# Kernel tuning notes

Measured on AMD Instinct MI355X. Metric: run time of the kernel, lower is better.

## Reference

```python
import jax, jax.numpy as jnp
import numpy as np

D = 768        # TEXT_DIM
N = 50         # seq len (h,w = 1,50 in source)
HEADS = 8
LABEL_SIZE = 50
B = 512
EPS_COS = 1e-8
EPS_LN = 1e-5


def _egce(x, w):
    # EGCE source not provided in repo snippet; implemented as ECA-style efficient
    # gated channel excitation: GAP over HW -> 1D conv (k=3) over channels -> sigmoid gate.
    gap = x.mean(axis=(2, 3))                      # [b, c]
    p = jnp.pad(gap, ((0, 0), (1, 1)))
    att = jax.nn.sigmoid(w[0] * p[:, :-2] + w[1] * p[:, 1:-1] + w[2] * p[:, 2:])
    return x * att[:, :, None, None]


def _lstm(x, Wih, Whh, bih, bhh):
    # PyTorch single-layer batch_first LSTM, gate order i,f,g,o, zero init state.
    b, n, d = x.shape
    xg = jnp.einsum('bnd,gd->bng', x, Wih) + bih + bhh   # [b, n, 4d]
    def step(carry, xt):
        h, c = carry
        g = xt + h @ Whh.T
        i, f, gg, o = jnp.split(g, 4, axis=-1)
        c = jax.nn.sigmoid(f) * c + jax.nn.sigmoid(i) * jnp.tanh(gg)
        h = jax.nn.sigmoid(o) * jnp.tanh(c)
        return (h, c), h
    h0 = jnp.zeros((b, d), x.dtype)
    _, ys = jax.lax.scan(step, (h0, h0), jnp.swapaxes(xg, 0, 1))
    return jnp.swapaxes(ys, 0, 1)


def _cross_attn(q_in, kv_in, qW, qb, kW, kb, vW, vb):
    b, n, d = q_in.shape
    dh = d // HEADS
    q = (q_in @ qW.T + qb).reshape(b, n, HEADS, dh).transpose(0, 2, 1, 3)
    k = (kv_in @ kW.T + kb).reshape(b, -1, HEADS, dh).transpose(0, 2, 1, 3)
    v = (kv_in @ vW.T + vb).reshape(b, -1, HEADS, dh).transpose(0, 2, 1, 3)
    attn = jax.nn.softmax(jnp.einsum('bhqd,bhkd->bhqk', q, k) * dh ** -0.5, axis=-1)
    # NOTE: faithful to source: einsum('bhqk,bhvd->bhqd') sums k and v INDEPENDENTLY
    out = jnp.einsum('bhqk,bhvd->bhqd', attn, v)
    return out.transpose(0, 2, 1, 3).reshape(b, n, d)


def _ln(x, g, b):
    m = x.mean(-1, keepdims=True)
    v = ((x - m) ** 2).mean(-1, keepdims=True)
    return (x - m) * jax.lax.rsqrt(v + EPS_LN) * g + b


def setup_inputs() -> dict:
    key = jax.random.key(0)
    ks = jax.random.split(key, 24)
    s = 0.02
    def w(k, shape):
        return jax.random.normal(k, shape, jnp.float32) * s
    vis_emb = w(ks[0], (LABEL_SIZE + 1, D)).at[LABEL_SIZE].set(0.0)
    ac_emb = w(ks[1], (LABEL_SIZE + 1, D)).at[LABEL_SIZE].set(0.0)
    inp = {
        'text_embedding': jax.random.normal(ks[2], (B, N, D), jnp.float32),
        'visual_ids': jax.random.randint(ks[3], (B, N), 0, LABEL_SIZE),
        'acoustic_ids': jax.random.randint(ks[4], (B, N), 0, LABEL_SIZE),
        'vis_emb': vis_emb,
        'ac_emb': ac_emb,
        'egce_w': w(ks[5], (3,)) + 0.3,
        'lstm_Wih': w(ks[6], (4 * D, D)),
        'lstm_Whh': w(ks[7], (4 * D, D)),
        'lstm_bih': jnp.zeros((4 * D,), jnp.float32),
        'lstm_bhh': jnp.zeros((4 * D,), jnp.float32),
        'ln_g': jnp.ones((D,), jnp.float32),
        'ln_b': jnp.zeros((D,), jnp.float32),
        'concat_W': w(ks[8], (D, 3 * D)),
        'concat_b': jnp.zeros((D,), jnp.float32),
        'hybrid_W': w(ks[9], (D, 3 * D)),
        'hybrid_b': jnp.zeros((D,), jnp.float32),
        # stacked cross-attention params, index 0 = cross_att_t, 1 = cross_att_a, 2 = cross_att_v
        'ca_qW': w(ks[10], (3, D, D)), 'ca_qb': w(ks[11], (3, D)),
        'ca_kW': w(ks[12], (3, D, D)), 'ca_kb': w(ks[13], (3, D)),
        'ca_vW': w(ks[14], (3, D, D)), 'ca_vb': w(ks[15], (3, D)),
    }
    return inp


def _forward(text_embedding, vis_emb, ac_emb, egce_w, lstm_Wih, lstm_Whh,
             lstm_bih, lstm_bhh, ln_g, ln_b, concat_W, concat_b, hybrid_W,
             hybrid_b, ca_qW, ca_qb, ca_kW, ca_kb, ca_vW, ca_vb,
             visual_ids, acoustic_ids):
    b, n, c = text_embedding.shape
    visual_ = jax.nn.relu(vis_emb[visual_ids])
    acoustic_ = ac_emb[acoustic_ids]
    # faithful reshape (NOT transpose) [b,n,c] -> [b,c,1,n] -> egce -> [b,n,c]
    text = _egce(text_embedding.reshape(b, c, 1, n), egce_w).reshape(b, n, c)
    visual_ = _egce(visual_.reshape(b, c, 1, n), egce_w).reshape(b, n, c)
    acoustic_ = _egce(acoustic_.reshape(b, c, 1, n), egce_w).reshape(b, n, c)

    # ---- AFI (vectorized over batch via masks instead of Python loop) ----
    def cos(x, y):
        xm, ym = x.mean(1), y.mean(1)
        nx = jnp.maximum(jnp.sqrt((xm * xm).sum(-1)), EPS_COS)
        ny = jnp.maximum(jnp.sqrt((ym * ym).sum(-1)), EPS_COS)
        return (xm * ym).sum(-1) / (nx * ny)
    rtv, rta, rva = cos(text, visual_), cos(text, acoustic_), cos(visual_, acoustic_)
    delta = (rtv + rta + rva) / 3.0
    joint = (rtv + rta + rva) / 3.0   # identical to delta in source
    cat = jnp.concatenate([text, visual_, acoustic_], axis=-1)  # [b,n,3d]
    f_concat = cat @ concat_W.T + concat_b
    f_hybrid = cat @ hybrid_W.T + hybrid_b
    tv = _cross_attn(text, visual_, ca_qW[0], ca_qb[0], ca_kW[0], ca_kb[0], ca_vW[0], ca_vb[0])
    ta = _cross_attn(text, acoustic_, ca_qW[1], ca_qb[1], ca_kW[1], ca_kb[1], ca_vW[1], ca_vb[1])
    va = _cross_attn(visual_, acoustic_, ca_qW[2], ca_qb[2], ca_kW[2], ca_kb[2], ca_vW[2], ca_vb[2])
    f_cross = (tv + ta + va) / 3.0
    m1 = ((rtv > delta) & (rta > delta) & (rva > delta))[:, None, None]
    m2 = (joint > delta)[:, None, None]
    fusion = jnp.where(m1, f_concat, jnp.where(m2, f_hybrid, f_cross))
    # dropout is identity in eval mode

    shift = _ln(fusion + text, ln_g, ln_b)
    out = _lstm(shift, lstm_Wih, lstm_Whh, lstm_bih, lstm_bhh) + text
    return out


def reference(text_embedding, visual_ids, acoustic_ids, vis_emb, ac_emb, egce_w,
              lstm_Wih, lstm_Whh, lstm_bih, lstm_bhh, ln_g, ln_b, concat_W,
              concat_b, hybrid_W, hybrid_b, ca_qW, ca_qb, ca_kW, ca_kb, ca_vW, ca_vb):
    return _forward(text_embedding, vis_emb, ac_emb, egce_w, lstm_Wih, lstm_Whh,
                    lstm_bih, lstm_bhh, ln_g, ln_b, concat_W, concat_b, hybrid_W,
                    hybrid_b, ca_qW, ca_qb, ca_kW, ca_kb, ca_vW, ca_vb,
                    visual_ids, acoustic_ids)
```

## Files before the change

kernel.cpp:

```cpp
#include <hip/hip_runtime.h>
#include <hip/hip_bf16.h>
#include <math.h>

#define B 512
#define N 50
#define D 768
#define G4 3072
#define BN (B*N)
#define FLAT (N*D)
#define TCH 10
#define NCHUNK (N/TCH)
#define KC 1536
#define CCH 6400

typedef __hip_bfloat16 bf16;
typedef short short8 __attribute__((ext_vector_type(8)));
typedef float floatx4 __attribute__((ext_vector_type(4)));

__device__ __forceinline__ float sigf(float x){ return 1.0f/(1.0f+expf(-x)); }
__device__ __forceinline__ float u2f(unsigned short u){ return __uint_as_float(((unsigned int)u)<<16); }
__device__ __forceinline__ unsigned short f2u(float f){ bf16 h=__float2bfloat16(f); return *(unsigned short*)&h; }

#define GLD16(g,l) __builtin_amdgcn_global_load_lds( \
    (const __attribute__((address_space(1))) unsigned int*)(g), \
    (__attribute__((address_space(3))) unsigned int*)(l), 16, 0, 0)

__global__ __launch_bounds__(256) void egce_fused(
    const float* __restrict__ text, const int* __restrict__ vid, const int* __restrict__ aid,
    const float* __restrict__ vemb, const float* __restrict__ aemb, const float* __restrict__ egw,
    float* __restrict__ att_t, unsigned short* __restrict__ catAB){
  __shared__ float buf[CCH];
  __shared__ float gt[D+2], gv[D+2], ga[D+2];
  __shared__ float attvS[D], attaS[D];
  __shared__ int vidS[N], aidS[N];
  int b=blockIdx.x, tid=threadIdx.x;
  if(tid<N){ vidS[tid]=vid[b*N+tid]; aidS[tid]=aid[b*N+tid]; }
  if(tid==0){ gt[0]=gv[0]=ga[0]=0.f; gt[D+1]=gv[D+1]=ga[D+1]=0.f; }
  __syncthreads();
  const float* tb = text + (size_t)b*FLAT;
  for(int c=0;c<6;c++){
    int j0=c*CCH;
    for(int it=0;it<25;it++) buf[it*256+tid]=tb[j0+it*256+tid];
    __syncthreads();
    if(tid<128){ float s=0.f; for(int p=0;p<50;p++) s+=buf[tid*50+p]; gt[c*128+tid+1]=s*(1.f/50.f); }
    __syncthreads();
    for(int it=0;it<25;it++){ int j=j0+it*256+tid; int n=j/D, d=j-n*D;
      float v=vemb[vidS[n]*D+d]; buf[it*256+tid]=v>0.f?v:0.f; }
    __syncthreads();
    if(tid<128){ float s=0.f; for(int p=0;p<50;p++) s+=buf[tid*50+p]; gv[c*128+tid+1]=s*(1.f/50.f); }
    __syncthreads();
    for(int it=0;it<25;it++){ int j=j0+it*256+tid; int n=j/D, d=j-n*D;
      buf[it*256+tid]=aemb[aidS[n]*D+d]; }
    __syncthreads();
    if(tid<128){ float s=0.f; for(int p=0;p<50;p++) s+=buf[tid*50+p]; ga[c*128+tid+1]=s*(1.f/50.f); }
    __syncthreads();
  }
  float w0=egw[0],w1=egw[1],w2=egw[2];
  for(int ch=tid;ch<D;ch+=256){
    att_t[(size_t)b*D+ch]=sigf(w0*gt[ch]+w1*gt[ch+1]+w2*gt[ch+2]);
    attvS[ch]=sigf(w0*gv[ch]+w1*gv[ch+1]+w2*gv[ch+2]);
    attaS[ch]=sigf(w0*ga[ch]+w1*ga[ch+1]+w2*ga[ch+2]);
  }
  __syncthreads();
  float va[3]={0,0,0}, aa[3]={0,0,0};
  for(int n=0;n<N;n++){
    int idv=vidS[n], ida=aidS[n];
    #pragma unroll
    for(int q=0;q<3;q++){
      int d=q*256+tid;
      int ch=(n*D+d)/50;
      float vv=vemb[idv*D+d]; vv=vv>0.f?vv:0.f;
      va[q]+=vv*attvS[ch];
      aa[q]+=aemb[ida*D+d]*attaS[ch];
    }
  }
  for(int q=0;q<3;q++){
    int d=q*256+tid;
    catAB[(size_t)b*KC+d]    =f2u(va[q]);
    catAB[(size_t)b*KC+D+d]  =f2u(aa[q]);
  }
}

__global__ __launch_bounds__(256) void prep_weights(
    const float* __restrict__ Wih, const float* __restrict__ Whh,
    const float* __restrict__ bih, const float* __restrict__ bhh,
    unsigned short* __restrict__ WihP, unsigned short* __restrict__ WhhP,
    float* __restrict__ bsum){
  int np = blockIdx.x;
  int dg = np>>2, g = np&3;
  size_t src = (size_t)(g*D+dg)*D;
  for(int k=threadIdx.x;k<D;k+=256){
    WihP[(size_t)np*D+k] = f2u(Wih[src+k]);
    WhhP[(size_t)np*D+k] = f2u(Whh[src+k]);
  }
  if(threadIdx.x==0) bsum[np] = bih[g*D+dg] + bhh[g*D+dg];
}

__global__ __launch_bounds__(256) void prep_fcross(
    const float* __restrict__ vW, const float* __restrict__ vb,
    unsigned short* __restrict__ WcB, float* __restrict__ fb){
  int n = blockIdx.x;
  const float* W0 = vW; const float* W1 = vW + D*D; const float* W2 = vW + 2*D*D;
  for(int k=threadIdx.x;k<D;k+=256){
    WcB[(size_t)n*KC + k]     = f2u(W0[(size_t)n*D+k]);
    WcB[(size_t)n*KC + D + k] = f2u(W1[(size_t)n*D+k] + W2[(size_t)n*D+k]);
  }
  if(threadIdx.x==0) fb[n] = 50.f*(vb[n]+vb[D+n]+vb[2*D+n]);
}

__global__ __launch_bounds__(256) void fcross_mfma(
    const unsigned short* __restrict__ catAB, const unsigned short* __restrict__ WcB,
    const float* __restrict__ fb, float* __restrict__ fcross){
  __shared__ unsigned short Ash[32*40];
  __shared__ unsigned short Bsh[64*40];
  int tid=threadIdx.x;
  int bx=blockIdx.x, by=blockIdx.y;
  int lane=tid&63, w=tid>>6;
  int l15=lane&15, lq=lane>>4;
  int arow=tid>>3, aseg=(tid&7)*4;
  int brow=tid>>2, bseg=(tid&3)*8;
  floatx4 acc0={},acc1={};
  const unsigned short* aG = catAB + (size_t)(by*32 + arow)*KC + aseg;
  const unsigned short* bG = WcB   + (size_t)(bx*64 + brow)*KC + bseg;
  for(int k0=0;k0<KC;k0+=32){
    *(uint2*)&Ash[arow*40 + aseg] = *(const uint2*)(aG + k0);
    *(uint4*)&Bsh[brow*40 + bseg] = *(const uint4*)(bG + k0);
    __syncthreads();
    short8 a0=*(const short8*)&Ash[l15*40 + lq*8];
    short8 a1=*(const short8*)&Ash[(16+l15)*40 + lq*8];
    short8 bb=*(const short8*)&Bsh[(w*16 + l15)*40 + lq*8];
    acc0=__builtin_amdgcn_mfma_f32_16x16x32_bf16(a0,bb,acc0,0,0,0);
    acc1=__builtin_amdgcn_mfma_f32_16x16x32_bf16(a1,bb,acc1,0,0,0);
    __syncthreads();
  }
  int n = bx*64 + w*16 + l15;
  float bias = fb[n];
  #pragma unroll
  for(int r=0;r<4;r++){
    int m0 = by*32 + lq*4 + r;
    fcross[(size_t)m0*D + n]      = (acc0[r] + bias)*(1.f/3.f);
    fcross[(size_t)(m0+16)*D + n] = (acc1[r] + bias)*(1.f/3.f);
  }
}

__global__ __launch_bounds__(256) void fuse_ln(
    const float* __restrict__ text, const float* __restrict__ att_t,
    const float* __restrict__ fcross, const float* __restrict__ lng,
    const float* __restrict__ lnb, bf16* __restrict__ shift){
  int row = blockIdx.x;
  int b = row/N, n = row - b*N;
  int tid=threadIdx.x;
  float v[3];
  for(int q=0;q<3;q++){
    int d=q*256+tid;
    int ch=(n*D+d)/50;
    v[q] = text[(size_t)row*D+d]*att_t[(size_t)b*D+ch] + fcross[(size_t)b*D+d];
  }
  __shared__ float red[256];
  red[tid]=v[0]+v[1]+v[2]; __syncthreads();
  for(int st=128;st>0;st>>=1){ if(tid<st) red[tid]+=red[tid+st]; __syncthreads(); }
  float m = red[0]*(1.f/768.f);
  __syncthreads();
  float s2=0.f;
  for(int q=0;q<3;q++){ float dl=v[q]-m; s2+=dl*dl; }
  red[tid]=s2; __syncthreads();
  for(int st=128;st>0;st>>=1){ if(tid<st) red[tid]+=red[tid+st]; __syncthreads(); }
  float var = red[0]*(1.f/768.f);
  float rs = 1.f/sqrtf(var+1e-5f);
  for(int q=0;q<3;q++){
    int d=q*256+tid;
    shift[(size_t)row*D+d]=__float2bfloat16((v[q]-m)*rs*lng[d]+lnb[d]);
  }
}

__global__ __launch_bounds__(256) void zero_init(float* __restrict__ cbuf, unsigned short* __restrict__ h0){
  size_t i=(size_t)blockIdx.x*256+threadIdx.x;
  if(i<(size_t)B*D){ cbuf[i]=0.f; h0[i]=0; }
}

__global__ __launch_bounds__(256) void xg_gemm_m97(
    const unsigned short* __restrict__ shift, const unsigned short* __restrict__ WihP,
    const float* __restrict__ bsum, unsigned short* __restrict__ xgc, int c0){
  __shared__ unsigned short Ash[128*32];
  __shared__ unsigned short Bsh[128*32];
  int tid=threadIdx.x;
  int bx=blockIdx.x, by=blockIdx.y;
  int lane=tid&63, w=tid>>6;
  int wm=w&1, wn=w>>1;
  int l15=lane&15, lq=lane>>4;
  int srow=tid>>2, scol=(tid&3)*8;
  int R0 = by*128 + srow;
  int b0 = R0/TCH, t0 = R0 - b0*TCH;
  int R1 = R0 + 64;
  int b1 = R1/TCH, t1 = R1 - b1*TCH;
  const unsigned short* aG0 = shift + ((size_t)b0*N + c0 + t0)*D + scol;
  const unsigned short* aG1 = shift + ((size_t)b1*N + c0 + t1)*D + scol;
  const unsigned short* bG0 = WihP + (size_t)(bx*128 + srow)*D + scol;
  const unsigned short* bG1 = WihP + (size_t)(bx*128 + srow + 64)*D + scol;
  unsigned short* aL0 = &Ash[srow*32 + scol];
  unsigned short* aL1 = &Ash[(srow+64)*32 + scol];
  unsigned short* bL0 = &Bsh[srow*32 + scol];
  unsigned short* bL1 = &Bsh[(srow+64)*32 + scol];
  floatx4 acc[4][4]={};
  for(int k0=0;k0<D;k0+=32){
    GLD16(aG0+k0, aL0);
    GLD16(aG1+k0, aL1);
    GLD16(bG0+k0, bL0);
    GLD16(bG1+k0, bL1);
    __syncthreads();
    short8 af[4], bf[4];
    #pragma unroll
    for(int i=0;i<4;i++){
      af[i]=*(const short8*)&Ash[(wm*64 + i*16 + l15)*32 + lq*8];
      bf[i]=*(const short8*)&Bsh[(wn*64 + i*16 + l15)*32 + lq*8];
    }
    #pragma unroll
    for(int mi=0;mi<4;mi++)
      #pragma unroll
      for(int ni=0;ni<4;ni++)
        acc[mi][ni]=__builtin_amdgcn_mfma_f32_16x16x32_bf16(af[mi],bf[ni],acc[mi][ni],0,0,0);
    __syncthreads();
  }
  #pragma unroll
  for(int ni=0;ni<4;ni++){
    int n = bx*128 + wn*64 + ni*16 + l15;
    float bs = bsum[n];
    #pragma unroll
    for(int mi=0;mi<4;mi++){
      #pragma unroll
      for(int r=0;r<4;r++){
        size_t m = (size_t)by*128 + wm*64 + mi*16 + lq*4 + r;
        xgc[m*G4 + n] = f2u(acc[mi][ni][r] + bs);
      }
    }
  }
}

__global__ __launch_bounds__(256) void lstm_step_mfma(
    const unsigned short* __restrict__ hprev, unsigned short* __restrict__ hnext,
    float* __restrict__ cbuf, const unsigned short* __restrict__ xgc,
    const unsigned short* __restrict__ WhhP,
    const float* __restrict__ text, const float* __restrict__ att_t,
    float* __restrict__ out, int t, int tin){
  __shared__ unsigned short Ash[32*40];
  __shared__ unsigned short Bsh[64*40];
  __shared__ float gbuf[32][65];
  int tid=threadIdx.x;
  int bx=blockIdx.x, by=blockIdx.y;
  int lane=tid&63, w=tid>>6;
  int l15=lane&15, lq=lane>>4;
  int arow=tid>>3, aseg=(tid&7)*4;
  int brow=tid>>2, bseg=(tid&3)*8;
  floatx4 acc0={},acc1={};
  const unsigned short* aG = hprev + (size_t)(by*32 + arow)*D + aseg;
  const unsigned short* bG = WhhP + (size_t)(bx*64 + brow)*D + bseg;
  for(int k0=0;k0<D;k0+=32){
    *(uint2*)&Ash[arow*40 + aseg] = *(const uint2*)(aG + k0);
    *(uint4*)&Bsh[brow*40 + bseg] = *(const uint4*)(bG + k0);
    __syncthreads();
    short8 a0=*(const short8*)&Ash[l15*40 + lq*8];
    short8 a1=*(const short8*)&Ash[(16+l15)*40 + lq*8];
    short8 bb=*(const short8*)&Bsh[(w*16 + l15)*40 + lq*8];
    acc0=__builtin_amdgcn_mfma_f32_16x16x32_bf16(a0,bb,acc0,0,0,0);
    acc1=__builtin_amdgcn_mfma_f32_16x16x32_bf16(a1,bb,acc1,0,0,0);
    __syncthreads();
  }
  {
    int n = w*16 + l15;
    #pragma unroll
    for(int r=0;r<4;r++){
      gbuf[lq*4+r][n]      = acc0[r];
      gbuf[16+lq*4+r][n]   = acc1[r];
    }
  }
  __syncthreads();
  for(int p=tid;p<512;p+=256){
    int bl=p>>4, dgl=p&15;
    int b=by*32+bl, dg=bx*16+dgl;
    size_t xr=((size_t)b*TCH + tin)*G4 + bx*64 + dgl*4;
    float gi=gbuf[bl][dgl*4+0] + u2f(xgc[xr+0]);
    float gf=gbuf[bl][dgl*4+1] + u2f(xgc[xr+1]);
    float gg=gbuf[bl][dgl*4+2] + u2f(xgc[xr+2]);
    float go=gbuf[bl][dgl*4+3] + u2f(xgc[xr+3]);
    float c_old=cbuf[(size_t)b*D+dg];
    float cn=sigf(gf)*c_old + sigf(gi)*tanhf(gg);
    float hn=sigf(go)*tanhf(cn);
    cbuf[(size_t)b*D+dg]=cn;
    hnext[(size_t)b*D+dg]=f2u(hn);
    size_t oidx=((size_t)b*N+t)*D+dg;
    int ch=(t*D+dg)/50;
    out[oidx]=hn + text[oidx]*att_t[(size_t)b*D+ch];
  }
}

extern "C" void kernel_launch(void* const* d_in, const int* in_sizes, int n_in,
                              void* d_out, int out_size, void* d_ws, size_t ws_size,
                              hipStream_t stream){
  const float* text=(const float*)d_in[0];
  const int*  vid =(const int*) d_in[1];
  const int*  aid =(const int*) d_in[2];
  const float* vemb=(const float*)d_in[3];
  const float* aemb=(const float*)d_in[4];
  const float* egw =(const float*)d_in[5];
  const float* Wih =(const float*)d_in[6];
  const float* Whh =(const float*)d_in[7];
  const float* bih =(const float*)d_in[8];
  const float* bhh =(const float*)d_in[9];
  const float* lng =(const float*)d_in[10];
  const float* lnb =(const float*)d_in[11];
  const float* vW  =(const float*)d_in[20];
  const float* vb  =(const float*)d_in[21];
  float* out = (float*)d_out;

  float* W = (float*)d_ws;
  const size_t S = (size_t)B*D;
  float* att_t = W;
  float* fcross= att_t + S;
  float* cbuf  = fcross + S;
  float* bsum  = cbuf + S;
  float* fb    = bsum + G4;
  unsigned short* WihP = (unsigned short*)(fb + D);
  unsigned short* WhhP = WihP + (size_t)G4*D;
  unsigned short* WcB  = WhhP + (size_t)G4*D;
  unsigned short* catAB= WcB + (size_t)D*KC;
  unsigned short* hA0  = catAB + (size_t)B*KC;
  unsigned short* hA1  = hA0 + S;
  bf16*  shift = (bf16*)(hA1 + S);
  unsigned short* xgc  = (unsigned short*)(shift + (size_t)BN*D);

  prep_weights<<<G4,256,0,stream>>>(Wih,Whh,bih,bhh,WihP,WhhP,bsum);
  prep_fcross<<<D,256,0,stream>>>(vW,vb,WcB,fb);
  egce_fused<<<B,256,0,stream>>>(text,vid,aid,vemb,aemb,egw,att_t,catAB);
  fcross_mfma<<<dim3(12,16),256,0,stream>>>(catAB,WcB,fb,fcross);
  fuse_ln<<<BN,256,0,stream>>>(text,att_t,fcross,lng,lnb,shift);
  zero_init<<<(unsigned)((S+255)/256),256,0,stream>>>(cbuf,hA0);

  int t=0;
  for(int c=0;c<NCHUNK;c++){
    xg_gemm_m97<<<dim3(24, 40),256,0,stream>>>((const unsigned short*)shift,WihP,bsum,xgc,c*TCH);
    for(int ti=0;ti<TCH;ti++,t++){
      unsigned short* hp = (t&1)? hA1 : hA0;
      unsigned short* hn = (t&1)? hA0 : hA1;
      lstm_step_mfma<<<dim3(48,16),256,0,stream>>>(hp,hn,cbuf,xgc,WhhP,text,att_t,out,t,ti);
    }
  }
}
```

Baseline: 1.252 ms.

## Replace per-step LSTM launches with persistent kernel using grid barrier

Measured after the change: 2.381 ms. +90.1%, slower.

```diff
diff --git a/kernel.cpp b/kernel.cpp
--- a/kernel.cpp
+++ b/kernel.cpp
@@ -8,8 +8,6 @@
 #define G4 3072
 #define BN (B*N)
 #define FLAT (N*D)
-#define TCH 10
-#define NCHUNK (N/TCH)
 #define KC 1536
 #define CCH 6400
 
@@ -20,10 +18,6 @@
 __device__ __forceinline__ float sigf(float x){ return 1.0f/(1.0f+expf(-x)); }
 __device__ __forceinline__ float u2f(unsigned short u){ return __uint_as_float(((unsigned int)u)<<16); }
 __device__ __forceinline__ unsigned short f2u(float f){ bf16 h=__float2bfloat16(f); return *(unsigned short*)&h; }
-
-#define GLD16(g,l) __builtin_amdgcn_global_load_lds( \
-    (const __attribute__((address_space(1))) unsigned int*)(g), \
-    (__attribute__((address_space(3))) unsigned int*)(l), 16, 0, 0)
 
 __global__ __launch_bounds__(256) void egce_fused(
     const float* __restrict__ text, const int* __restrict__ vid, const int* __restrict__ aid,
@@ -173,123 +167,140 @@
   }
 }
 
-__global__ __launch_bounds__(256) void zero_init(float* __restrict__ cbuf, unsigned short* __restrict__ h0){
-  size_t i=(size_t)blockIdx.x*256+threadIdx.x;
-  if(i<(size_t)B*D){ cbuf[i]=0.f; h0[i]=0; }
-}
-
-__global__ __launch_bounds__(256) void xg_gemm_m97(
+__global__ __launch_bounds__(256) void zero_bar(int* __restrict__ bar){
+  bar[threadIdx.x] = 0;
+}
+
+__global__ __launch_bounds__(512) void lstm_persist(
     const unsigned short* __restrict__ shift, const unsigned short* __restrict__ WihP,
-    const float* __restrict__ bsum, unsigned short* __restrict__ xgc, int c0){
-  __shared__ unsigned short Ash[128*32];
-  __shared__ unsigned short Bsh[128*32];
-  int tid=threadIdx.x;
-  int bx=blockIdx.x, by=blockIdx.y;
-  int lane=tid&63, w=tid>>6;
-  int wm=w&1, wn=w>>1;
-  int l15=lane&15, lq=lane>>4;
-  int srow=tid>>2, scol=(tid&3)*8;
-  int R0 = by*128 + srow;
-  int b0 = R0/TCH, t0 = R0 - b0*TCH;
-  int R1 = R0 + 64;
-  int b1 = R1/TCH, t1 = R1 - b1*TCH;
-  const unsigned short* aG0 = shift + ((size_t)b0*N + c0 + t0)*D + scol;
-  const unsigned short* aG1 = shift + ((size_t)b1*N + c0 + t1)*D + scol;
-  const unsigned short* bG0 = WihP + (size_t)(bx*128 + srow)*D + scol;
-  const unsigned short* bG1 = WihP + (size_t)(bx*128 + srow + 64)*D + scol;
-  unsigned short* aL0 = &Ash[srow*32 + scol];
-  unsigned short* aL1 = &Ash[(srow+64)*32 + scol];
-  unsigned short* bL0 = &Bsh[srow*32 + scol];
-  unsigned short* bL1 = &Bsh[(srow+64)*32 + scol];
-  floatx4 acc[4][4]={};
-  for(int k0=0;k0<D;k0+=32){
-    GLD16(aG0+k0, aL0);
-    GLD16(aG1+k0, aL1);
-    GLD16(bG0+k0, bL0);
-    GLD16(bG1+k0, bL1);
-    __syncthreads();
-    short8 af[4], bf[4];
+    const unsigned short* __restrict__ WhhP, const float* __restrict__ bsum,
+    const float* __restrict__ text, const float* __restrict__ att_t,
+    unsigned short* __restrict__ h0b, unsigned short* __restrict__ h1b,
+    float* __restrict__ out, int* __restrict__ bar){
+  __shared__ unsigned short Wsl[2*2*3840];
+  const int tid = threadIdx.x;
+  const int bid = blockIdx.x;
+  const int k8 = bid & 7, u = bid >> 3;
+  const int gy = u & 7;
+  const int gx = (u >> 3) + (k8 << 2);
+  const int lane = tid & 63, w = tid >> 6;
+  const int wn = w & 1, wm = w >> 1;
+  const int l15 = lane & 15, lq = lane >> 4;
+
+  const int arrA = (tid < 384) ? 0 : 1;
+  const int sA   = (tid < 384) ? tid : tid - 384;
+  const int rlA = sA >> 2, cA = sA & 3;
+  const unsigned short* srcA = (arrA ? WihP : WhhP) + (size_t)(gx*96 + rlA)*D + cA*8;
+  const int dA = arrA*3840 + rlA*40 + cA*8;
+  const bool hasB = (tid < 256);
+  const int sB = tid + 128;
+  const int rlB = sB >> 2, cB = sB & 3;
+  const unsigned short* srcB = WihP + (size_t)(gx*96 + rlB)*D + cB*8;
+  const int dB = 3840 + rlB*40 + cB*8;
+
+  const int mrow = gy*64 + wm*16 + l15;
+  int rdh[3], rdi[3];
+  #pragma unroll
+  for(int fi=0;fi<3;fi++){
+    int rl = wn*48 + fi*16 + l15;
+    rdh[fi] = rl*40 + lq*8;
+    rdi[fi] = 3840 + rl*40 + lq*8;
+  }
+  int dgv[3]; floatx4 bs[3];
+  #pragma unroll
+  for(int fi=0;fi<3;fi++){
+    int nb = gx*96 + wn*48 + fi*16 + lq*4;
+    dgv[fi] = nb >> 2;
+    bs[fi] = *(const floatx4*)&bsum[nb];
+  }
+
+  float cst[3] = {0.f, 0.f, 0.f};
+
+  #pragma unroll 1
+  for(int t=0;t<50;++t){
+    const unsigned short* hR = (t&1) ? h1b : h0b;
+    unsigned short* hW = (t&1) ? h0b : h1b;
+    const unsigned short* sP = shift + ((size_t)mrow*N + t)*D + lq*8;
+    const unsigned short* hP = hR + (size_t)mrow*D + lq*8;
+
+    floatx4 acc[3] = {};
+
+    uint4 rA = *(const uint4*)(srcA);
+    uint4 rB = {}; if(hasB) rB = *(const uint4*)(srcB);
+    short8 sfC = *(const short8*)(sP);
+    short8 hfC = {}; if(t) hfC = *(const short8*)(hP);
+    *(uint4*)&Wsl[dA] = rA;
+    if(hasB) *(uint4*)&Wsl[dB] = rB;
+    __syncthreads();
+
     #pragma unroll
-    for(int i=0;i<4;i++){
-      af[i]=*(const short8*)&Ash[(wm*64 + i*16 + l15)*32 + lq*8];
-      bf[i]=*(const short8*)&Bsh[(wn*64 + i*16 + l15)*32 + lq*8];
+    for(int kk=0;kk<24;++kk){
+      const int bo = (kk&1)*7680;
+      uint4 nA = {}; uint4 nB = {}; short8 sfN = {}; short8 hfN = {};
+      if(kk < 23){
+        nA = *(const uint4*)(srcA + (kk+1)*32);
+        if(hasB) nB = *(const uint4*)(srcB + (kk+1)*32);
+        sfN = *(const short8*)(sP + (kk+1)*32);
+        if(t) hfN = *(const short8*)(hP + (kk+1)*32);
+      }
+      #pragma unroll
+      for(int fi=0;fi<3;fi++){
+        short8 wi = *(const short8*)&Wsl[bo + rdi[fi]];
+        acc[fi] = __builtin_amdgcn_mfma_f32_16x16x32_bf16(wi, sfC, acc[fi], 0,0,0);
+      }
+      if(t){
+        #pragma unroll
+        for(int fi=0;fi<3;fi++){
+          short8 wh = *(const short8*)&Wsl[bo + rdh[fi]];
+          acc[fi] = __builtin_amdgcn_mfma_f32_16x16x32_bf16(wh, hfC, acc[fi], 0,0,0);
+        }
+      }
+      if(kk < 23){
+        const int nx = 7680 - bo;
+        *(uint4*)&Wsl[nx + dA] = nA;
+        if(hasB) *(uint4*)&Wsl[nx + dB] = nB;
+        sfC = sfN; hfC = hfN;
+      }
+      __syncthreads();
     }
+
+    size_t tb = ((size_t)mrow*N + t)*D;
     #pragma unroll
-    for(int mi=0;mi<4;mi++)
-      #pragma unroll
-      for(int ni=0;ni<4;ni++)
-        acc[mi][ni]=__builtin_amdgcn_mfma_f32_16x16x32_bf16(af[mi],bf[ni],acc[mi][ni],0,0,0);
-    __syncthreads();
-  }
-  #pragma unroll
-  for(int ni=0;ni<4;ni++){
-    int n = bx*128 + wn*64 + ni*16 + l15;
-    float bs = bsum[n];
-    #pragma unroll
-    for(int mi=0;mi<4;mi++){
-      #pragma unroll
-      for(int r=0;r<4;r++){
-        size_t m = (size_t)by*128 + wm*64 + mi*16 + lq*4 + r;
-        xgc[m*G4 + n] = f2u(acc[mi][ni][r] + bs);
-      }
+    for(int fi=0;fi<3;fi++){
+      float gi = acc[fi][0] + bs[fi][0];
+      float gf = acc[fi][1] + bs[fi][1];
+      float gg = acc[fi][2] + bs[fi][2];
+      float go = acc[fi][3] + bs[fi][3];
+      float cn = sigf(gf)*cst[fi] + sigf(gi)*tanhf(gg);
+      float hn = sigf(go)*tanhf(cn);
+      cst[fi] = cn;
+      int dg = dgv[fi];
+      hW[(size_t)mrow*D + dg] = f2u(hn);
+      int ch = (t*D + dg)/50;
+      out[tb + dg] = hn + text[tb + dg]*att_t[(size_t)mrow*D + ch];
     }
-  }
-}
-
-__global__ __launch_bounds__(256) void lstm_step_mfma(
-    const unsigned short* __restrict__ hprev, unsigned short* __restrict__ hnext,
-    float* __restrict__ cbuf, const unsigned short* __restrict__ xgc,
-    const unsigned short* __restrict__ WhhP,
-    const float* __restrict__ text, const float* __restrict__ att_t,
-    float* __restrict__ out, int t, int tin){
-  __shared__ unsigned short Ash[32*40];
-  __shared__ unsigned short Bsh[64*40];
-  __shared__ float gbuf[32][65];
-  int tid=threadIdx.x;
-  int bx=blockIdx.x, by=blockIdx.y;
-  int lane=tid&63, w=tid>>6;
-  int l15=lane&15, lq=lane>>4;
-  int arow=tid>>3, aseg=(tid&7)*4;
-  int brow=tid>>2, bseg=(tid&3)*8;
-  floatx4 acc0={},acc1={};
-  const unsigned short* aG = hprev + (size_t)(by*32 + arow)*D + aseg;
-  const unsigned short* bG = WhhP + (size_t)(bx*64 + brow)*D + bseg;
-  for(int k0=0;k0<D;k0+=32){
-    *(uint2*)&Ash[arow*40 + aseg] = *(const uint2*)(aG + k0);
-    *(uint4*)&Bsh[brow*40 + bseg] = *(const uint4*)(bG + k0);
-    __syncthreads();
-    short8 a0=*(const short8*)&Ash[l15*40 + lq*8];
-    short8 a1=*(const short8*)&Ash[(16+l15)*40 + lq*8];
-    short8 bb=*(const short8*)&Bsh[(w*16 + l15)*40 + lq*8];
-    acc0=__builtin_amdgcn_mfma_f32_16x16x32_bf16(a0,bb,acc0,0,0,0);
-    acc1=__builtin_amdgcn_mfma_f32_16x16x32_bf16(a1,bb,acc1,0,0,0);
-    __syncthreads();
-  }
-  {
-    int n = w*16 + l15;
-    #pragma unroll
-    for(int r=0;r<4;r++){
-      gbuf[lq*4+r][n]      = acc0[r];
-      gbuf[16+lq*4+r][n]   = acc1[r];
+
+    if(t < 49){
+      __syncthreads();
+      if(tid == 0){
+        __threadfence();
+        __hip_atomic_store(&bar[bid], t+1, __ATOMIC_RELEASE, __HIP_MEMORY_SCOPE_AGENT);
+      }
+      if(w == 0){
+        int i0 = lane*4;
+        while(true){
+          int a0 = __hip_atomic_load(&bar[i0+0], __ATOMIC_RELAXED, __HIP_MEMORY_SCOPE_AGENT);
+          int a1 = __hip_atomic_load(&bar[i0+1], __ATOMIC_RELAXED, __HIP_MEMORY_SCOPE_AGENT);
+          int a2 = __hip_atomic_load(&bar[i0+2], __ATOMIC_RELAXED, __HIP_MEMORY_SCOPE_AGENT);
+          int a3 = __hip_atomic_load(&bar[i0+3], __ATOMIC_RELAXED, __HIP_MEMORY_SCOPE_AGENT);
+          int mn = min(min(a0,a1), min(a2,a3));
+          if(__all(mn >= t+1)) break;
+          __builtin_amdgcn_s_sleep(2);
+        }
+        __threadfence();
+      }
+      __syncthreads();
     }
-  }
-  __syncthreads();
-  for(int p=tid;p<512;p+=256){
-    int bl=p>>4, dgl=p&15;
-    int b=by*32+bl, dg=bx*16+dgl;
-    size_t xr=((size_t)b*TCH + tin)*G4 + bx*64 + dgl*4;
-    float gi=gbuf[bl][dgl*4+0] + u2f(xgc[xr+0]);
-    float gf=gbuf[bl][dgl*4+1] + u2f(xgc[xr+1]);
-    float gg=gbuf[bl][dgl*4+2] + u2f(xgc[xr+2]);
-    float go=gbuf[bl][dgl*4+3] + u2f(xgc[xr+3]);
-    float c_old=cbuf[(size_t)b*D+dg];
-    float cn=sigf(gf)*c_old + sigf(gi)*tanhf(gg);
-    float hn=sigf(go)*tanhf(cn);
-    cbuf[(size_t)b*D+dg]=cn;
-    hnext[(size_t)b*D+dg]=f2u(hn);
-    size_t oidx=((size_t)b*N+t)*D+dg;
-    int ch=(t*D+dg)/50;
-    out[oidx]=hn + text[oidx]*att_t[(size_t)b*D+ch];
   }
 }
 
@@ -326,22 +337,14 @@
   unsigned short* hA0  = catAB + (size_t)B*KC;
   unsigned short* hA1  = hA0 + S;
   bf16*  shift = (bf16*)(hA1 + S);
-  unsigned short* xgc  = (unsigned short*)(shift + (size_t)BN*D);
+  int* bar = (int*)cbuf;
 
   prep_weights<<<G4,256,0,stream>>>(Wih,Whh,bih,bhh,WihP,WhhP,bsum);
   prep_fcross<<<D,256,0,stream>>>(vW,vb,WcB,fb);
   egce_fused<<<B,256,0,stream>>>(text,vid,aid,vemb,aemb,egw,att_t,catAB);
   fcross_mfma<<<dim3(12,16),256,0,stream>>>(catAB,WcB,fb,fcross);
   fuse_ln<<<BN,256,0,stream>>>(text,att_t,fcross,lng,lnb,shift);
-  zero_init<<<(unsigned)((S+255)/256),256,0,stream>>>(cbuf,hA0);
-
-  int t=0;
-  for(int c=0;c<NCHUNK;c++){
-    xg_gemm_m97<<<dim3(24, 40),256,0,stream>>>((const unsigned short*)shift,WihP,bsum,xgc,c*TCH);
-    for(int ti=0;ti<TCH;ti++,t++){
-      unsigned short* hp = (t&1)? hA1 : hA0;
-      unsigned short* hn = (t&1)? hA0 : hA1;
-      lstm_step_mfma<<<dim3(48,16),256,0,stream>>>(hp,hn,cbuf,xgc,WhhP,text,att_t,out,t,ti);
-    }
-  }
-}
+  zero_bar<<<1,256,0,stream>>>(bar);
+  lstm_persist<<<256,512,0,stream>>>((const unsigned short*)shift,WihP,WhhP,bsum,
+                                     text,att_t,hA0,hA1,out,bar);
+}
```

## Fuse LSTM input projection into per-step recurrent GEMM with concatenated weights

Applied to the files above, without the earlier changes.

Result: no change. 1.268 ms (+1.2%).

```diff
diff --git a/kernel.cpp b/kernel.cpp
--- a/kernel.cpp
+++ b/kernel.cpp
@@ -6,10 +6,9 @@
 #define N 50
 #define D 768
 #define G4 3072
+#define KCAT 1536
 #define BN (B*N)
 #define FLAT (N*D)
-#define TCH 10
-#define NCHUNK (N/TCH)
 #define KC 1536
 #define CCH 6400
 
@@ -20,10 +19,6 @@
 __device__ __forceinline__ float sigf(float x){ return 1.0f/(1.0f+expf(-x)); }
 __device__ __forceinline__ float u2f(unsigned short u){ return __uint_as_float(((unsigned int)u)<<16); }
 __device__ __forceinline__ unsigned short f2u(float f){ bf16 h=__float2bfloat16(f); return *(unsigned short*)&h; }
-
-#define GLD16(g,l) __builtin_amdgcn_global_load_lds( \
-    (const __attribute__((address_space(1))) unsigned int*)(g), \
-    (__attribute__((address_space(3))) unsigned int*)(l), 16, 0, 0)
 
 __global__ __launch_bounds__(256) void egce_fused(
     const float* __restrict__ text, const int* __restrict__ vid, const int* __restrict__ aid,
@@ -84,14 +79,13 @@
 __global__ __launch_bounds__(256) void prep_weights(
     const float* __restrict__ Wih, const float* __restrict__ Whh,
     const float* __restrict__ bih, const float* __restrict__ bhh,
-    unsigned short* __restrict__ WihP, unsigned short* __restrict__ WhhP,
-    float* __restrict__ bsum){
+    unsigned short* __restrict__ Wcat, float* __restrict__ bsum){
   int np = blockIdx.x;
   int dg = np>>2, g = np&3;
   size_t src = (size_t)(g*D+dg)*D;
   for(int k=threadIdx.x;k<D;k+=256){
-    WihP[(size_t)np*D+k] = f2u(Wih[src+k]);
-    WhhP[(size_t)np*D+k] = f2u(Whh[src+k]);
+    Wcat[(size_t)np*KCAT + k]     = f2u(Whh[src+k]);
+    Wcat[(size_t)np*KCAT + D + k] = f2u(Wih[src+k]);
   }
   if(threadIdx.x==0) bsum[np] = bih[g*D+dg] + bhh[g*D+dg];
 }
@@ -173,123 +167,94 @@
   }
 }
 
-__global__ __launch_bounds__(256) void zero_init(float* __restrict__ cbuf, unsigned short* __restrict__ h0){
-  size_t i=(size_t)blockIdx.x*256+threadIdx.x;
-  if(i<(size_t)B*D){ cbuf[i]=0.f; h0[i]=0; }
-}
-
-__global__ __launch_bounds__(256) void xg_gemm_m97(
-    const unsigned short* __restrict__ shift, const unsigned short* __restrict__ WihP,
-    const float* __restrict__ bsum, unsigned short* __restrict__ xgc, int c0){
-  __shared__ unsigned short Ash[128*32];
-  __shared__ unsigned short Bsh[128*32];
-  int tid=threadIdx.x;
-  int bx=blockIdx.x, by=blockIdx.y;
-  int lane=tid&63, w=tid>>6;
-  int wm=w&1, wn=w>>1;
-  int l15=lane&15, lq=lane>>4;
-  int srow=tid>>2, scol=(tid&3)*8;
-  int R0 = by*128 + srow;
-  int b0 = R0/TCH, t0 = R0 - b0*TCH;
-  int R1 = R0 + 64;
-  int b1 = R1/TCH, t1 = R1 - b1*TCH;
-  const unsigned short* aG0 = shift + ((size_t)b0*N + c0 + t0)*D + scol;
-  const unsigned short* aG1 = shift + ((size_t)b1*N + c0 + t1)*D + scol;
-  const unsigned short* bG0 = WihP + (size_t)(bx*128 + srow)*D + scol;
-  const unsigned short* bG1 = WihP + (size_t)(bx*128 + srow + 64)*D + scol;
-  unsigned short* aL0 = &Ash[srow*32 + scol];
-  unsigned short* aL1 = &Ash[(srow+64)*32 + scol];
-  unsigned short* bL0 = &Bsh[srow*32 + scol];
-  unsigned short* bL1 = &Bsh[(srow+64)*32 + scol];
-  floatx4 acc[4][4]={};
-  for(int k0=0;k0<D;k0+=32){
-    GLD16(aG0+k0, aL0);
-    GLD16(aG1+k0, aL1);
-    GLD16(bG0+k0, bL0);
-    GLD16(bG1+k0, bL1);
-    __syncthreads();
-    short8 af[4], bf[4];
-    #pragma unroll
-    for(int i=0;i<4;i++){
-      af[i]=*(const short8*)&Ash[(wm*64 + i*16 + l15)*32 + lq*8];
-      bf[i]=*(const short8*)&Bsh[(wn*64 + i*16 + l15)*32 + lq*8];
+__global__ __launch_bounds__(256) void lstm_fused(
+    const unsigned short* __restrict__ shift, const unsigned short* __restrict__ Wcat,
+    const float* __restrict__ bsum, const unsigned short* __restrict__ hprev,
+    unsigned short* __restrict__ hnext, float* __restrict__ cbuf,
+    const float* __restrict__ text, const float* __restrict__ att_t,
+    float* __restrict__ out, int t){
+  __shared__ unsigned short Ab[2][64*40];
+  __shared__ unsigned short Bb[2][128*40];
+  const int tid=threadIdx.x, bx=blockIdx.x, by=blockIdx.y;
+  const int lane=tid&63, w=tid>>6, l15=lane&15, lq=lane>>4;
+
+  const int sra = tid>>2, ca=(tid&3)*8;
+  const int arow = sra&31, ah = sra>>5;
+  const int dA = sra*40 + ca;
+  const int b_a = by*32 + arow;
+  const unsigned short* hThr = hprev + (size_t)b_a*D + ah*32 + ca;
+  const unsigned short* xThr = shift + ((size_t)b_a*N + t)*D + ah*32 + ca;
+
+  const int sr0 = tid>>2,        c0=(tid&3)*8;
+  const int sr1 = (tid+256)>>2,  c1=(tid&3)*8;
+  const int br0 = sr0&63, bh0 = sr0>>6;
+  const int br1 = sr1&63, bh1 = sr1>>6;
+  const unsigned short* bThr0 = Wcat + (size_t)(bx*64+br0)*KCAT + bh0*32 + c0;
+  const unsigned short* bThr1 = Wcat + (size_t)(bx*64+br1)*KCAT + bh1*32 + c1;
+  const int dB0 = sr0*40 + c0, dB1 = sr1*40 + c1;
+
+  const int kbase  = t ? 0 : 768;
+  const int nIters = t ? 24 : 12;
+
+  floatx4 acc0={}, acc1={};
+
+  {
+    const unsigned short* ap = (kbase<768) ? (hThr + kbase) : (xThr + (kbase-768));
+    uint4 pA  = *(const uint4*)ap;
+    uint4 pB0 = *(const uint4*)(bThr0 + kbase);
+    uint4 pB1 = *(const uint4*)(bThr1 + kbase);
+    *(uint4*)&Ab[0][dA]  = pA;
+    *(uint4*)&Bb[0][dB0] = pB0;
+    *(uint4*)&Bb[0][dB1] = pB1;
+  }
+  __syncthreads();
+
+  #pragma unroll 2
+  for(int it=0; it<nIters; ++it){
+    const int cur = it&1;
+    uint4 nA, nB0, nB1;
+    const bool more = (it+1 < nIters);
+    if(more){
+      int kg = kbase + (it+1)*64;
+      const unsigned short* ap = (kg<768) ? (hThr + kg) : (xThr + (kg-768));
+      nA  = *(const uint4*)ap;
+      nB0 = *(const uint4*)(bThr0 + kg);
+      nB1 = *(const uint4*)(bThr1 + kg);
     }
-    #pragma unroll
-    for(int mi=0;mi<4;mi++)
-      #pragma unroll
-      for(int ni=0;ni<4;ni++)
-        acc[mi][ni]=__builtin_amdgcn_mfma_f32_16x16x32_bf16(af[mi],bf[ni],acc[mi][ni],0,0,0);
-    __syncthreads();
-  }
+    short8 Wf0 = *(const short8*)&Bb[cur][(w*16+l15)*40 + lq*8];
+    short8 Wf1 = *(const short8*)&Bb[cur][(64 + w*16+l15)*40 + lq*8];
+    short8 X00 = *(const short8*)&Ab[cur][(l15)*40 + lq*8];
+    short8 X10 = *(const short8*)&Ab[cur][(16+l15)*40 + lq*8];
+    short8 X01 = *(const short8*)&Ab[cur][(32+l15)*40 + lq*8];
+    short8 X11 = *(const short8*)&Ab[cur][(48+l15)*40 + lq*8];
+    acc0 = __builtin_amdgcn_mfma_f32_16x16x32_bf16(Wf0, X00, acc0, 0,0,0);
+    acc1 = __builtin_amdgcn_mfma_f32_16x16x32_bf16(Wf0, X10, acc1, 0,0,0);
+    acc0 = __builtin_amdgcn_mfma_f32_16x16x32_bf16(Wf1, X01, acc0, 0,0,0);
+    acc1 = __builtin_amdgcn_mfma_f32_16x16x32_bf16(Wf1, X11, acc1, 0,0,0);
+    if(more){
+      *(uint4*)&Ab[cur^1][dA]  = nA;
+      *(uint4*)&Bb[cur^1][dB0] = nB0;
+      *(uint4*)&Bb[cur^1][dB1] = nB1;
+    }
+    __syncthreads();
+  }
+
+  const int nb = bx*64 + w*16 + lq*4;
+  const int dg = nb>>2;
+  floatx4 bs = *(const floatx4*)&bsum[nb];
   #pragma unroll
-  for(int ni=0;ni<4;ni++){
-    int n = bx*128 + wn*64 + ni*16 + l15;
-    float bs = bsum[n];
-    #pragma unroll
-    for(int mi=0;mi<4;mi++){
-      #pragma unroll
-      for(int r=0;r<4;r++){
-        size_t m = (size_t)by*128 + wm*64 + mi*16 + lq*4 + r;
-        xgc[m*G4 + n] = f2u(acc[mi][ni][r] + bs);
-      }
-    }
-  }
-}
-
-__global__ __launch_bounds__(256) void lstm_step_mfma(
-    const unsigned short* __restrict__ hprev, unsigned short* __restrict__ hnext,
-    float* __restrict__ cbuf, const unsigned short* __restrict__ xgc,
-    const unsigned short* __restrict__ WhhP,
-    const float* __restrict__ text, const float* __restrict__ att_t,
-    float* __restrict__ out, int t, int tin){
-  __shared__ unsigned short Ash[32*40];
-  __shared__ unsigned short Bsh[64*40];
-  __shared__ float gbuf[32][65];
-  int tid=threadIdx.x;
-  int bx=blockIdx.x, by=blockIdx.y;
-  int lane=tid&63, w=tid>>6;
-  int l15=lane&15, lq=lane>>4;
-  int arow=tid>>3, aseg=(tid&7)*4;
-  int brow=tid>>2, bseg=(tid&3)*8;
-  floatx4 acc0={},acc1={};
-  const unsigned short* aG = hprev + (size_t)(by*32 + arow)*D + aseg;
-  const unsigned short* bG = WhhP + (size_t)(bx*64 + brow)*D + bseg;
-  for(int k0=0;k0<D;k0+=32){
-    *(uint2*)&Ash[arow*40 + aseg] = *(const uint2*)(aG + k0);
-    *(uint4*)&Bsh[brow*40 + bseg] = *(const uint4*)(bG + k0);
-    __syncthreads();
-    short8 a0=*(const short8*)&Ash[l15*40 + lq*8];
-    short8 a1=*(const short8*)&Ash[(16+l15)*40 + lq*8];
-    short8 bb=*(const short8*)&Bsh[(w*16 + l15)*40 + lq*8];
-    acc0=__builtin_amdgcn_mfma_f32_16x16x32_bf16(a0,bb,acc0,0,0,0);
-    acc1=__builtin_amdgcn_mfma_f32_16x16x32_bf16(a1,bb,acc1,0,0,0);
-    __syncthreads();
-  }
-  {
-    int n = w*16 + l15;
-    #pragma unroll
-    for(int r=0;r<4;r++){
-      gbuf[lq*4+r][n]      = acc0[r];
-      gbuf[16+lq*4+r][n]   = acc1[r];
-    }
-  }
-  __syncthreads();
-  for(int p=tid;p<512;p+=256){
-    int bl=p>>4, dgl=p&15;
-    int b=by*32+bl, dg=bx*16+dgl;
-    size_t xr=((size_t)b*TCH + tin)*G4 + bx*64 + dgl*4;
-    float gi=gbuf[bl][dgl*4+0] + u2f(xgc[xr+0]);
-    float gf=gbuf[bl][dgl*4+1] + u2f(xgc[xr+1]);
-    float gg=gbuf[bl][dgl*4+2] + u2f(xgc[xr+2]);
-    float go=gbuf[bl][dgl*4+3] + u2f(xgc[xr+3]);
-    float c_old=cbuf[(size_t)b*D+dg];
-    float cn=sigf(gf)*c_old + sigf(gi)*tanhf(gg);
-    float hn=sigf(go)*tanhf(cn);
-    cbuf[(size_t)b*D+dg]=cn;
-    hnext[(size_t)b*D+dg]=f2u(hn);
-    size_t oidx=((size_t)b*N+t)*D+dg;
-    int ch=(t*D+dg)/50;
-    out[oidx]=hn + text[oidx]*att_t[(size_t)b*D+ch];
+  for(int mf=0; mf<2; ++mf){
+    floatx4 a = mf ? acc1 : acc0;
+    int b = by*32 + mf*16 + l15;
+    float gi=a[0]+bs[0], gf=a[1]+bs[1], gg=a[2]+bs[2], go=a[3]+bs[3];
+    float co = t ? cbuf[(size_t)b*D+dg] : 0.f;
+    float cn = sigf(gf)*co + sigf(gi)*tanhf(gg);
+    float hn = sigf(go)*tanhf(cn);
+    cbuf[(size_t)b*D+dg] = cn;
+    hnext[(size_t)b*D+dg] = f2u(hn);
+    int ch = (t*D+dg)/50;
+    size_t oi = ((size_t)b*N + t)*D + dg;
+    out[oi] = hn + text[oi]*att_t[(size_t)b*D+ch];
   }
 }
 
@@ -319,29 +284,23 @@
   float* cbuf  = fcross + S;
   float* bsum  = cbuf + S;
   float* fb    = bsum + G4;
-  unsigned short* WihP = (unsigned short*)(fb + D);
-  unsigned short* WhhP = WihP + (size_t)G4*D;
-  unsigned short* WcB  = WhhP + (size_t)G4*D;
+  unsigned short* Wcat = (unsigned short*)(fb + D);
+  unsigned short* WcB  = Wcat + (size_t)G4*KCAT;
   unsigned short* catAB= WcB + (size_t)D*KC;
   unsigned short* hA0  = catAB + (size_t)B*KC;
   unsigned short* hA1  = hA0 + S;
   bf16*  shift = (bf16*)(hA1 + S);
-  unsigned short* xgc  = (unsigned short*)(shift + (size_t)BN*D);
-
-  prep_weights<<<G4,256,0,stream>>>(Wih,Whh,bih,bhh,WihP,WhhP,bsum);
+
+  prep_weights<<<G4,256,0,stream>>>(Wih,Whh,bih,bhh,Wcat,bsum);
   prep_fcross<<<D,256,0,stream>>>(vW,vb,WcB,fb);
   egce_fused<<<B,256,0,stream>>>(text,vid,aid,vemb,aemb,egw,att_t,catAB);
   fcross_mfma<<<dim3(12,16),256,0,stream>>>(catAB,WcB,fb,fcross);
   fuse_ln<<<BN,256,0,stream>>>(text,att_t,fcross,lng,lnb,shift);
-  zero_init<<<(unsigned)((S+255)/256),256,0,stream>>>(cbuf,hA0);
-
-  int t=0;
-  for(int c=0;c<NCHUNK;c++){
-    xg_gemm_m97<<<dim3(24, 40),256,0,stream>>>((const unsigned short*)shift,WihP,bsum,xgc,c*TCH);
-    for(int ti=0;ti<TCH;ti++,t++){
-      unsigned short* hp = (t&1)? hA1 : hA0;
-      unsigned short* hn = (t&1)? hA0 : hA1;
-      lstm_step_mfma<<<dim3(48,16),256,0,stream>>>(hp,hn,cbuf,xgc,WhhP,text,att_t,out,t,ti);
-    }
-  }
-}
+
+  for(int t=0;t<N;t++){
+    unsigned short* hp = (t&1)? hA1 : hA0;
+    unsigned short* hn = (t&1)? hA0 : hA1;
+    lstm_fused<<<dim3(48,16),256,0,stream>>>((const unsigned short*)shift,Wcat,bsum,
+                                             hp,hn,cbuf,text,att_t,out,t);
+  }
+}
```
